# Kernel tuning notes

Hardware: AMD Instinct MI355X
Metric: run time of the kernel (lower is better)

## Reference

```python
import jax, jax.numpy as jnp
import numpy as np

L, H, C = 2, 8, 128          # layers, heads, hidden_channels
D = C // H                   # head dim
NPAT, NICD, NNDC = 50000, 591, 2042
OUT = 90
E = 250000                   # edges per relation
# edge relations as (src_type, dst_type); node types: 0=patient, 1=icd, 2=ndc
ETYPES = [(0, 1), (1, 0), (0, 2), (2, 0)]


def _seg_softmax(logits, seg, n):
    # softmax over edges grouped by destination node (PyG `softmax`)
    m = jax.ops.segment_max(logits, seg, num_segments=n)
    e = jnp.exp(logits - m[seg])
    s = jax.ops.segment_sum(e, seg, num_segments=n)
    return e / s[seg]


def setup_inputs() -> dict:
    key = jax.random.key(0)
    ks = jax.random.split(key, 24)
    s = 1.0 / np.sqrt(C)
    n = lambda k, shape, sc: jax.random.normal(k, shape, dtype=jnp.float32) * sc
    return {
        "x_patient": n(ks[0], (NPAT, C), 1.0),
        "w_in_patient": n(ks[1], (C, C), s),
        "b_in_patient": jnp.zeros((C,), jnp.float32),
        "emb_icd": n(ks[2], (NICD, C), 0.1),
        "emb_ndc": n(ks[3], (NNDC, C), 0.1),
        "kw": n(ks[4], (L, 3, C, C), s), "kb": jnp.zeros((L, 3, C), jnp.float32),
        "qw": n(ks[5], (L, 3, C, C), s), "qb": jnp.zeros((L, 3, C), jnp.float32),
        "vw": n(ks[6], (L, 3, C, C), s), "vb": jnp.zeros((L, 3, C), jnp.float32),
        "aw": n(ks[7], (L, 3, C, C), s), "ab": jnp.zeros((L, 3, C), jnp.float32),
        "skip": jnp.ones((L, 3), jnp.float32),
        "a_rel": n(ks[8], (L, 4, H, D, D), 1.0 / np.sqrt(D)),
        "m_rel": n(ks[9], (L, 4, H, D, D), 1.0 / np.sqrt(D)),
        "p_rel": jnp.ones((L, 4, H), jnp.float32),
        "w_out": n(ks[10], (C, OUT), s),
        "b_out": jnp.zeros((OUT,), jnp.float32),
        "x_icd": jnp.arange(NICD, dtype=jnp.int32),
        "x_ndc": jnp.arange(NNDC, dtype=jnp.int32),
        "src_pi": jax.random.randint(ks[11], (E,), 0, NPAT, dtype=jnp.int32),
        "dst_pi": jax.random.randint(ks[12], (E,), 0, NICD, dtype=jnp.int32),
        "src_ip": jax.random.randint(ks[13], (E,), 0, NICD, dtype=jnp.int32),
        "dst_ip": jax.random.randint(ks[14], (E,), 0, NPAT, dtype=jnp.int32),
        "src_pn": jax.random.randint(ks[15], (E,), 0, NPAT, dtype=jnp.int32),
        "dst_pn": jax.random.randint(ks[16], (E,), 0, NNDC, dtype=jnp.int32),
        "src_np": jax.random.randint(ks[17], (E,), 0, NNDC, dtype=jnp.int32),
        "dst_np": jax.random.randint(ks[18], (E,), 0, NPAT, dtype=jnp.int32),
    }


def reference(x_patient, w_in_patient, b_in_patient, emb_icd, emb_ndc,
              kw, kb, qw, qb, vw, vb, aw, ab, skip,
              a_rel, m_rel, p_rel, w_out, b_out,
              x_icd, x_ndc,
              src_pi, dst_pi, src_ip, dst_ip, src_pn, dst_pn, src_np, dst_np):
    edges = [(src_pi, dst_pi), (src_ip, dst_ip), (src_pn, dst_pn), (src_np, dst_np)]
    sizes = [NPAT, NICD, NNDC]
    # per-type input projection / embedding + relu
    x = [jax.nn.relu(x_patient @ w_in_patient + b_in_patient),
         jax.nn.relu(emb_icd[x_icd]),
         jax.nn.relu(emb_ndc[x_ndc])]
    scale = 1.0 / np.sqrt(D)
    for l in range(L):
        k = [(x[t] @ kw[l, t] + kb[l, t]).reshape(-1, H, D) for t in range(3)]
        q = [(x[t] @ qw[l, t] + qb[l, t]).reshape(-1, H, D) for t in range(3)]
        v = [(x[t] @ vw[l, t] + vb[l, t]).reshape(-1, H, D) for t in range(3)]
        agg = [jnp.zeros((sizes[t], H, D), x[0].dtype) for t in range(3)]
        for r, (st, dt) in enumerate(ETYPES):
            src, dst = edges[r]
            kr = jnp.einsum('nhd,hde->nhe', k[st], a_rel[l, r])  # relation key transform
            vr = jnp.einsum('nhd,hde->nhe', v[st], m_rel[l, r])  # relation msg transform
            alpha = jnp.sum(q[dt][dst] * kr[src], axis=-1) * p_rel[l, r] * scale  # [E,H]
            alpha = _seg_softmax(alpha, dst, sizes[dt])
            agg[dt] = agg[dt] + jax.ops.segment_sum(vr[src] * alpha[:, :, None], dst, num_segments=sizes[dt])
        new_x = []
        for t in range(3):
            o = jax.nn.gelu(agg[t].reshape(-1, C)) @ aw[l, t] + ab[l, t]
            a = jax.nn.sigmoid(skip[l, t])
            new_x.append(a * o + (1.0 - a) * x[t])  # learned skip (dims match)
        x = new_x
    return jax.nn.sigmoid(x[0] @ w_out + b_out)
```

## Files before the change

### kernel.cpp

```cpp
#include <hip/hip_runtime.h>
#include <math.h>

#define CDIM  128
#define NHEAD 8
#define DHEAD 16
#define NPAT  50000
#define NICD  591
#define NNDC  2042
#define OUTN  90
#define NEDGE 250000
#define NLAYER 2
#define ALC   640

#define OFF0  0
#define OFF1  (NICD)
#define OFF2  (NICD + NPAT)
#define OFF3  (NICD + NPAT + NNDC)
#define NTOT  (NICD + NPAT + NNDC + NPAT)

#define LDP 40
#define CTILE 72
#define LOG2E 1.4426950408889634f

typedef __attribute__((ext_vector_type(8))) short bf16x8;
typedef __attribute__((ext_vector_type(4))) float f32x4;

__device__ __forceinline__ float gelu_tanh(float x) {
    float x3 = x * x * x;
    return 0.5f * x * (1.0f + tanhf(0.7978845608028654f * (x + 0.044715f * x3)));
}
__device__ __forceinline__ float b2f(unsigned short u) {
    union { unsigned int i; float f; } v; v.i = ((unsigned int)u) << 16; return v.f;
}
__device__ __forceinline__ unsigned short f2b(float f) {
    union { float ff; unsigned int i; } v; v.ff = f;
    unsigned int i = v.i;
    return (unsigned short)((i + 0x7FFFu + ((i >> 16) & 1u)) >> 16);
}
__device__ __forceinline__ float2 b2x2(unsigned int u) {
    union { unsigned int i; float f; } lo, hi;
    lo.i = u << 16; hi.i = u & 0xFFFF0000u;
    return make_float2(lo.f, hi.f);
}

__global__ __launch_bounds__(256) void gemm_xs(
    const void* __restrict__ Ap, int a_mode, int lda,
    const unsigned short* __restrict__ Wt, const float* __restrict__ bias,
    void* __restrict__ Cp, int c_mode, int ldc,
    int M, int N, int act, int ntile,
    const unsigned short* __restrict__ xold, int ldx,
    const float* __restrict__ skipv, int skipidx)
{
    __shared__ unsigned short Al[64 * LDP];
    __shared__ unsigned short Bl[64 * LDP];
    __shared__ unsigned short Cst[64 * CTILE];
    int nwg = gridDim.x;
    int orig = blockIdx.x;
    int qq = nwg >> 3, rr = nwg & 7;
    int xcd = orig & 7, idx = orig >> 3;
    int wgid = (xcd < rr ? xcd * (qq + 1) : rr * (qq + 1) + (xcd - rr) * qq) + idx;
    int bm = (wgid / ntile) * 64, bn = (wgid % ntile) * 64;

    int t = threadIdx.x;
    int lane = t & 63, w = t >> 6;
    int wr = w >> 1, wc = w & 1;
    int quad = lane >> 4, lm = lane & 15;
    f32x4 acc[2][2] = {};
    const int srow = t >> 2;
    const int skq  = (t & 3) * 8;

    for (int k0 = 0; k0 < 128; k0 += 32) {
        {
            int row = bm + srow;
            uint4 u = make_uint4(0, 0, 0, 0);
            if (a_mode == 0) {
                if (row < M)
                    u = *(const uint4*)((const unsigned short*)Ap + (size_t)row * lda + k0 + skq);
            } else {
                float f[8] = {0.f,0.f,0.f,0.f,0.f,0.f,0.f,0.f};
                if (row < M) {
                    const float4* ap = (const float4*)((const float*)Ap + (size_t)row * lda + k0 + skq);
                    float4 u0 = ap[0], u1 = ap[1];
                    f[0]=u0.x; f[1]=u0.y; f[2]=u0.z; f[3]=u0.w;
                    f[4]=u1.x; f[5]=u1.y; f[6]=u1.z; f[7]=u1.w;
                }
                unsigned short v[8];
                for (int i = 0; i < 8; i++) v[i] = f2b(f[i]);
                u = *(uint4*)v;
            }
            *(uint4*)&Al[srow * LDP + skq] = u;
        }
        {
            int n = bn + srow;
            uint4 u = make_uint4(0, 0, 0, 0);
            if (n < N) u = *(const uint4*)(Wt + (size_t)n * 128 + k0 + skq);
            *(uint4*)&Bl[srow * LDP + skq] = u;
        }
        __syncthreads();
        bf16x8 af[2], bfr[2];
        #pragma unroll
        for (int i = 0; i < 2; i++) {
            af[i]  = *(const bf16x8*)&Al[(wr * 32 + i * 16 + lm) * LDP + quad * 8];
            bfr[i] = *(const bf16x8*)&Bl[(wc * 32 + i * 16 + lm) * LDP + quad * 8];
        }
        acc[0][0] = __builtin_amdgcn_mfma_f32_16x16x32_bf16(af[0], bfr[0], acc[0][0], 0, 0, 0);
        acc[0][1] = __builtin_amdgcn_mfma_f32_16x16x32_bf16(af[0], bfr[1], acc[0][1], 0, 0, 0);
        acc[1][0] = __builtin_amdgcn_mfma_f32_16x16x32_bf16(af[1], bfr[0], acc[1][0], 0, 0, 0);
        acc[1][1] = __builtin_amdgcn_mfma_f32_16x16x32_bf16(af[1], bfr[1], acc[1][1], 0, 0, 0);
        __syncthreads();
    }

    float aSk = 0.f, oneM = 0.f;
    if (skipv) {
        float sv = skipv[skipidx];
        aSk = 1.0f / (1.0f + expf(-sv));
        oneM = 1.0f - aSk;
    }
    if (c_mode == 0) {
        #pragma unroll
        for (int tm = 0; tm < 2; tm++)
        #pragma unroll
        for (int tn = 0; tn < 2; tn++)
        #pragma unroll
        for (int r = 0; r < 4; r++) {
            int lrow = wr * 32 + tm * 16 + quad * 4 + r;
            int lcol = wc * 32 + tn * 16 + lm;
            int row = bm + lrow, col = bn + lcol;
            float v = acc[tm][tn][r] + (bias ? bias[col] : 0.f);
            if (act == 1) v = fmaxf(v, 0.f);
            if (skipv && row < M) v = aSk * v + oneM * b2f(xold[(size_t)row * ldx + col]);
            Cst[lrow * CTILE + lcol] = f2b(v);
        }
        __syncthreads();
        int row = t >> 2, seg = (t & 3) * 16;
        if (bm + row < M) {
            unsigned short* dst = (unsigned short*)Cp + (size_t)(bm + row) * ldc + bn + seg;
            *(uint4*)dst       = *(const uint4*)&Cst[row * CTILE + seg];
            *(uint4*)(dst + 8) = *(const uint4*)&Cst[row * CTILE + seg + 8];
        }
    } else {
        #pragma unroll
        for (int tm = 0; tm < 2; tm++)
        #pragma unroll
        for (int tn = 0; tn < 2; tn++)
        #pragma unroll
        for (int r = 0; r < 4; r++) {
            int row = bm + wr * 32 + tm * 16 + quad * 4 + r;
            int col = bn + wc * 32 + tn * 16 + lm;
            if (row >= M || col >= N) continue;
            float v = acc[tm][tn][r] + (bias ? bias[col] : 0.f);
            if (act == 1) v = fmaxf(v, 0.f);
            else if (act == 2) v = 1.0f / (1.0f + expf(-v));
            ((float*)Cp)[(size_t)row * ldc + col] = v;
        }
    }
}

__global__ __launch_bounds__(256) void wprep_all(
    const float* __restrict__ qw, const float* __restrict__ aw,
    const float* __restrict__ w_in, const float* __restrict__ w_out,
    unsigned short* __restrict__ Wb0, unsigned short* __restrict__ Wb1,
    unsigned short* __restrict__ Wb2, unsigned short* __restrict__ Wtaw,
    unsigned short* __restrict__ Wtin, unsigned short* __restrict__ Wtout)
{
    __shared__ float tile[32][33];
    int z = blockIdx.z;
    const float* s; unsigned short* d; int N = 128;
    if (z < 2)       { s = qw + (size_t)z * 3 * 16384;              d = Wb0 + (size_t)z * 640 * 128; }
    else if (z < 4)  { s = qw + 16384 + (size_t)(z - 2) * 3 * 16384; d = Wb1 + (size_t)(z - 2) * 384 * 128; }
    else if (z < 6)  { s = qw + 2 * 16384 + (size_t)(z - 4) * 3 * 16384; d = Wb2 + (size_t)(z - 4) * 384 * 128; }
    else if (z < 12) { s = aw + (size_t)(z - 6) * 16384;            d = Wtaw + (size_t)(z - 6) * 16384; }
    else if (z == 12){ s = w_in;  d = Wtin; }
    else             { s = w_out; d = Wtout; N = OUTN; }
    int k0 = blockIdx.x * 32, n0 = blockIdx.y * 32;
    int tx = threadIdx.x & 31, ty = threadIdx.x >> 5;
    for (int i = 0; i < 32; i += 8) {
        int k = k0 + ty + i, n = n0 + tx;
        tile[ty + i][tx] = (k < 128 && n < N) ? s[(size_t)k * N + n] : 0.f;
    }
    __syncthreads();
    for (int i = 0; i < 32; i += 8) {
        int n = n0 + ty + i, k = k0 + tx;
        if (n < N && k < 128) d[(size_t)n * 128 + k] = f2b(tile[tx][ty + i]);
    }
}

__global__ __launch_bounds__(256) void wcomp_kernel(
    const float* __restrict__ kw, const float* __restrict__ vw,
    const float* __restrict__ a_rel, const float* __restrict__ m_rel,
    const float* __restrict__ kb, const float* __restrict__ vb,
    unsigned short* __restrict__ Wb0, unsigned short* __restrict__ Wb1,
    unsigned short* __restrict__ Wb2,
    float* __restrict__ bb0, float* __restrict__ bb1, float* __restrict__ bb2)
{
    int s = blockIdx.x;
    int l = s >> 3, j = s & 7;
    int t, isV, r, rowoff, nw;
    unsigned short* Wb; float* bb;
    switch (j) {
      case 0: t=0; isV=0; r=0; Wb=Wb0; bb=bb0; rowoff=128; nw=640; break;
      case 1: t=0; isV=1; r=0; Wb=Wb0; bb=bb0; rowoff=256; nw=640; break;
      case 2: t=0; isV=0; r=2; Wb=Wb0; bb=bb0; rowoff=384; nw=640; break;
      case 3: t=0; isV=1; r=2; Wb=Wb0; bb=bb0; rowoff=512; nw=640; break;
      case 4: t=1; isV=0; r=1; Wb=Wb1; bb=bb1; rowoff=128; nw=384; break;
      case 5: t=1; isV=1; r=1; Wb=Wb1; bb=bb1; rowoff=256; nw=384; break;
      case 6: t=2; isV=0; r=3; Wb=Wb2; bb=bb2; rowoff=128; nw=384; break;
      default:t=2; isV=1; r=3; Wb=Wb2; bb=bb2; rowoff=256; nw=384; break;
    }
    const float* W = (isV ? vw : kw) + (size_t)(l * 3 + t) * 16384;
    const float* A = (isV ? m_rel : a_rel) + (size_t)(l * 4 + r) * 2048;
    const float* B = (isV ? vb : kb) + (size_t)(l * 3 + t) * 128;
    unsigned short* dst = Wb + (size_t)l * nw * 128 + (size_t)rowoff * 128;
    float* bdst = bb + (size_t)l * nw + rowoff;
    int n = threadIdx.x & 127;
    int kh = threadIdx.x >> 7;
    int h = n >> 4, e = n & 15;
    float Ar[16];
    #pragma unroll
    for (int d = 0; d < 16; d++) Ar[d] = A[h * 256 + d * 16 + e];
    for (int k = kh * 64; k < kh * 64 + 64; k++) {
        float acc = 0.f;
        const float* wr = W + (size_t)k * 128 + h * 16;
        #pragma unroll
        for (int d = 0; d < 16; d++) acc += wr[d] * Ar[d];
        dst[(size_t)n * 128 + k] = f2b(acc);
    }
    if (kh == 0) {
        float acc = 0.f;
        const float* br = B + h * 16;
        #pragma unroll
        for (int d = 0; d < 16; d++) acc += br[d] * Ar[d];
        bdst[n] = acc;
    }
}

__global__ void biasq_kernel(const float* __restrict__ qb,
                             float* __restrict__ bb0, float* __restrict__ bb1,
                             float* __restrict__ bb2) {
    int t = blockIdx.x * blockDim.x + threadIdx.x;
    if (t >= 6 * 128) return;
    int g = t >> 7, c = t & 127;
    int l = g / 3, ty = g % 3;
    float v = qb[g * 128 + c];
    if (ty == 0) bb0[l * 640 + c] = v;
    else if (ty == 1) bb1[l * 384 + c] = v;
    else bb2[l * 384 + c] = v;
}

__global__ __launch_bounds__(256) void hist4_kernel(
    const int* __restrict__ d0, const int* __restrict__ d1,
    const int* __restrict__ d2, const int* __restrict__ d3,
    int* __restrict__ deg)
{
    __shared__ int lh[2048];
    int rel = blockIdx.y;
    int t = threadIdx.x;
    const int* dp = (rel == 0) ? d0 : (rel == 1) ? d1 : (rel == 2) ? d2 : d3;
    int off = (rel == 0) ? OFF0 : (rel == 1) ? OFF1 : (rel == 2) ? OFF2 : OFF3;
    if (rel == 1 || rel == 3) {
        for (int e = blockIdx.x * 256 + t; e < NEDGE; e += gridDim.x * 256)
            atomicAdd(&deg[off + dp[e]], 1);
    } else {
        int nb = (rel == 0) ? NICD : NNDC;
        for (int i = t; i < nb; i += 256) lh[i] = 0;
        __syncthreads();
        for (int e = blockIdx.x * 256 + t; e < NEDGE; e += gridDim.x * 256)
            atomicAdd(&lh[dp[e]], 1);
        __syncthreads();
        for (int i = t; i < nb; i += 256) {
            int v = lh[i];
            if (v) atomicAdd(&deg[off + i], v);
        }
    }
}

__global__ __launch_bounds__(256) void scanA_kernel(
    const int* __restrict__ deg, int* __restrict__ part, int n)
{
    __shared__ int red[256];
    int b = blockIdx.x, t = threadIdx.x;
    int base = b * 1024 + t * 4;
    int s = 0;
    if (base + 3 < n) {
        int4 v = *(const int4*)(deg + base);
        s = v.x + v.y + v.z + v.w;
    } else {
        for (int i = 0; i < 4; i++) if (base + i < n) s += deg[base + i];
    }
    red[t] = s;
    __syncthreads();
    for (int o = 128; o; o >>= 1) { if (t < o) red[t] += red[t + o]; __syncthreads(); }
    if (t == 0) part[b] = red[0];
}

__global__ __launch_bounds__(128) void scanB_kernel(int* __restrict__ part, int nb)
{
    __shared__ int s[256];
    int t = threadIdx.x;
    for (int i = t; i < nb; i += 128) s[i] = part[i];
    __syncthreads();
    if (t == 0) { int run = 0; for (int i = 0; i < nb; i++) { int v = s[i]; s[i] = run; run += v; } }
    __syncthreads();
    for (int i = t; i < nb; i += 128) part[i] = s[i];
}

__global__ __launch_bounds__(256) void scanC_kernel(
    const int* __restrict__ deg, const int* __restrict__ part,
    int* __restrict__ rp0, int* __restrict__ rp1,
    int* __restrict__ rp2, int* __restrict__ rp3,
    int* __restrict__ cursor, int n)
{
    __shared__ int red[256];
    int b = blockIdx.x, t = threadIdx.x;
    int base = b * 1024 + t * 4;
    int v[4] = {0, 0, 0, 0};
    if (base + 3 < n) {
        int4 q = *(const int4*)(deg + base);
        v[0] = q.x; v[1] = q.y; v[2] = q.z; v[3] = q.w;
    } else {
        for (int i = 0; i < 4; i++) if (base + i < n) v[i] = deg[base + i];
    }
    red[t] = v[0] + v[1] + v[2] + v[3];
    __syncthreads();
    for (int off = 1; off < 256; off <<= 1) {
        int y = (t >= off) ? red[t - off] : 0;
        __syncthreads();
        red[t] += y;
        __syncthreads();
    }
    int run = part[b] + ((t == 0) ? 0 : red[t - 1]);
    for (int i = 0; i < 4; i++) {
        int g = base + i;
        if (g < n) {
            cursor[g] = run;
            int r, loc;
            if      (g < OFF1) { r = 0; loc = g; }
            else if (g < OFF2) { r = 1; loc = g - OFF1; }
            else if (g < OFF3) { r = 2; loc = g - OFF2; }
            else               { r = 3; loc = g - OFF3; }
            int Sl = run - r * NEDGE;
            ((r == 0) ? rp0 : (r == 1) ? rp1 : (r == 2) ? rp2 : rp3)[loc] = Sl;
            run += v[i];
        }
    }
    if (b == 0 && t == 0) {
        rp0[NICD] = NEDGE; rp1[NPAT] = NEDGE; rp2[NNDC] = NEDGE; rp3[NPAT] = NEDGE;
    }
}

__global__ __launch_bounds__(256) void scatter_pack_kernel(
    const int* __restrict__ s0, const int* __restrict__ d0,
    const int* __restrict__ s1, const int* __restrict__ d1,
    const int* __restrict__ s2, const int* __restrict__ d2,
    const int* __restrict__ s3, const int* __restrict__ d3,
    int* __restrict__ cursor, unsigned int* __restrict__ es)
{
    __shared__ int lcnt[2048];
    __shared__ int lbase[2048];
    int rel = blockIdx.y;
    int t = threadIdx.x;
    const int* sp = (rel == 0) ? s0 : (rel == 1) ? s1 : (rel == 2) ? s2 : s3;
    const int* dp = (rel == 0) ? d0 : (rel == 1) ? d1 : (rel == 2) ? d2 : d3;
    int off = (rel == 0) ? OFF0 : (rel == 1) ? OFF1 : (rel == 2) ? OFF2 : OFF3;
    if (rel == 1 || rel == 3) {
        for (int e = blockIdx.x * 256 + t; e < NEDGE; e += gridDim.x * 256) {
            int d = dp[e];
            int p = atomicAdd(&cursor[off + d], 1);
            es[p] = ((unsigned int)sp[e] << 16) | (unsigned int)d;
        }
    } else {
        int nb = (rel == 0) ? NICD : NNDC;
        int per = (NEDGE + gridDim.x - 1) / gridDim.x;
        int e0 = blockIdx.x * per, e1 = min(e0 + per, NEDGE);
        for (int i = t; i < nb; i += 256) lcnt[i] = 0;
        __syncthreads();
        for (int e = e0 + t; e < e1; e += 256) atomicAdd(&lcnt[dp[e]], 1);
        __syncthreads();
        for (int i = t; i < nb; i += 256) {
            int c = lcnt[i];
            lbase[i] = c ? atomicAdd(&cursor[off + i], c) : 0;
            lcnt[i] = 0;
        }
        __syncthreads();
        for (int e = e0 + t; e < e1; e += 256) {
            int d = dp[e];
            int p = lbase[d] + atomicAdd(&lcnt[d], 1);
            es[p] = ((unsigned int)sp[e] << 16) | (unsigned int)d;
        }
    }
}

__global__ void gather_relu2_kernel(
    const float* __restrict__ embA, const int* __restrict__ idxA,
    unsigned short* __restrict__ outA, int nA,
    const float* __restrict__ embB, const int* __restrict__ idxB,
    unsigned short* __restrict__ outB, int nB)
{
    int t = blockIdx.x * blockDim.x + threadIdx.x;
    int totA = nA * CDIM;
    if (t < totA) {
        int r = t >> 7, c = t & 127;
        outA[t] = f2b(fmaxf(embA[(size_t)idxA[r] * CDIM + c], 0.f));
    } else if (t < totA + nB * CDIM) {
        int u = t - totA;
        int r = u >> 7, c = u & 127;
        outB[u] = f2b(fmaxf(embB[(size_t)idxB[r] * CDIM + c], 0.f));
    }
}

__device__ __forceinline__ float dot16_bf(const unsigned short* a,
                                          const unsigned short* b) {
    const uint4* ap = (const uint4*)a;
    const uint4* bp = (const uint4*)b;
    uint4 a0 = ap[0], a1 = ap[1], b0 = bp[0], b1 = bp[1];
    unsigned int au[8] = {a0.x, a0.y, a0.z, a0.w, a1.x, a1.y, a1.z, a1.w};
    unsigned int bu[8] = {b0.x, b0.y, b0.z, b0.w, b1.x, b1.y, b1.z, b1.w};
    float acc = 0.f;
    #pragma unroll
    for (int j = 0; j < 8; j++) {
        float2 x = b2x2(au[j]), y = b2x2(bu[j]);
        acc += x.x * y.x + x.y * y.y;
    }
    return acc;
}

__device__ __forceinline__ float dot16_q(uint4 a0, uint4 a1,
                                         const unsigned short* b) {
    const uint4* bp = (const uint4*)b;
    uint4 b0 = bp[0], b1 = bp[1];
    unsigned int au[8] = {a0.x, a0.y, a0.z, a0.w, a1.x, a1.y, a1.z, a1.w};
    unsigned int bu[8] = {b0.x, b0.y, b0.z, b0.w, b1.x, b1.y, b1.z, b1.w};
    float acc = 0.f;
    #pragma unroll
    for (int j = 0; j < 8; j++) {
        float2 x = b2x2(au[j]), y = b2x2(bu[j]);
        acc += x.x * y.x + x.y * y.y;
    }
    return acc;
}

__global__ __launch_bounds__(256) void seg_fused_kernel(
    const int* __restrict__ rpA, const unsigned int* __restrict__ esA,
    const unsigned short* __restrict__ qA, int ldqA,
    const unsigned short* __restrict__ krA, const unsigned short* __restrict__ vrA, int ldsA,
    const float* __restrict__ prelA, float* __restrict__ alphaA,
    unsigned short* __restrict__ aggA, int ndA,
    const int* __restrict__ rpB, const unsigned int* __restrict__ esB,
    const unsigned short* __restrict__ qB, int ldqB,
    const unsigned short* __restrict__ krB, const unsigned short* __restrict__ vrB, int ldsB,
    const float* __restrict__ prelB, float* __restrict__ alphaB,
    unsigned short* __restrict__ aggB, int ndB)
{
    __shared__ float wred[4][8];
    __shared__ float sinv[8];
    __shared__ float p3f[4][64][2];
    __shared__ float wl[ALC * NHEAD];
    __shared__ unsigned short sl[ALC];
    int rel = blockIdx.y;
    int n = blockIdx.x;
    const int* rp            = rel ? rpB : rpA;
    const unsigned int* es   = rel ? esB : esA;
    const unsigned short* q  = rel ? qB : qA;
    int ldq                  = rel ? ldqB : ldqA;
    const unsigned short* kr = rel ? krB : krA;
    const unsigned short* vr = rel ? vrB : vrA;
    int ldsrc                = rel ? ldsB : ldsA;
    const float* prel        = rel ? prelB : prelA;
    float* alpha             = rel ? alphaB : alphaA;
    unsigned short* agg      = rel ? aggB : aggA;
    int nd                   = rel ? ndB : ndA;
    if (n >= nd) return;

    int r0 = rp[n], deg = rp[n + 1] - r0;
    int t = threadIdx.x;
    int h = t & 7, j = t >> 3;
    int lane = t & 63, wv = t >> 6;
    const unsigned short* qrow = q + (size_t)n * ldq + h * DHEAD;
    uint4 qa = ((const uint4*)qrow)[0], qb = ((const uint4*)qrow)[1];
    float ph = prel[h] * 0.25f * LOG2E;

    if (deg <= ALC) {
        for (int i = t; i < deg; i += 256) sl[i] = (unsigned short)(es[r0 + i] >> 16);
        __syncthreads();

        float mx = -1e30f;
        int i = j;
        for (; i + 96 < deg; i += 128) {
            int s0 = sl[i], s1 = sl[i + 32], s2 = sl[i + 64], s3 = sl[i + 96];
            float a0 = dot16_q(qa, qb, kr + (size_t)s0 * ldsrc + h * DHEAD) * ph;
            float a1 = dot16_q(qa, qb, kr + (size_t)s1 * ldsrc + h * DHEAD) * ph;
            float a2 = dot16_q(qa, qb, kr + (size_t)s2 * ldsrc + h * DHEAD) * ph;
            float a3 = dot16_q(qa, qb, kr + (size_t)s3 * ldsrc + h * DHEAD) * ph;
            wl[(i)      * NHEAD + h] = a0;
            wl[(i + 32) * NHEAD + h] = a1;
            wl[(i + 64) * NHEAD + h] = a2;
            wl[(i + 96) * NHEAD + h] = a3;
            mx = fmaxf(mx, fmaxf(fmaxf(a0, a1), fmaxf(a2, a3)));
        }
        for (; i < deg; i += 32) {
            int s0 = sl[i];
            float a = dot16_q(qa, qb, kr + (size_t)s0 * ldsrc + h * DHEAD) * ph;
            wl[i * NHEAD + h] = a;
            mx = fmaxf(mx, a);
        }
        mx = fmaxf(mx, __shfl_xor(mx, 8));
        mx = fmaxf(mx, __shfl_xor(mx, 16));
        mx = fmaxf(mx, __shfl_xor(mx, 32));
        if (lane < 8) wred[wv][h] = mx;
        __syncthreads();
        float m = fmaxf(fmaxf(wred[0][h], wred[1][h]), fmaxf(wred[2][h], wred[3][h]));
        __syncthreads();

        float sm = 0.f;
        for (i = j; i < deg; i += 32) {
            float e = exp2f(wl[i * NHEAD + h] - m);
            wl[i * NHEAD + h] = e;
            sm += e;
        }
        sm += __shfl_xor(sm, 8);
        sm += __shfl_xor(sm, 16);
        sm += __shfl_xor(sm, 32);
        if (lane < 8) wred[wv][h] = sm;
        __syncthreads();
        if (t < 8) {
            float s = wred[0][t] + wred[1][t] + wred[2][t] + wred[3][t];
            sinv[t] = (s > 0.f) ? 1.0f / s : 0.f;
        }
        __syncthreads();

        int g = t >> 6, l = t & 63;
        int hh = l >> 3;
        float acc0 = 0.f, acc1 = 0.f;
        i = g;
        for (; i + 28 < deg; i += 32) {
            int e0 = sl[i],      e1 = sl[i + 4],  e2 = sl[i + 8],  e3 = sl[i + 12];
            int e4 = sl[i + 16], e5 = sl[i + 20], e6 = sl[i + 24], e7 = sl[i + 28];
            unsigned int u0 = *(const unsigned int*)(vr + (size_t)e0 * ldsrc + 2 * l);
            unsigned int u1 = *(const unsigned int*)(vr + (size_t)e1 * ldsrc + 2 * l);
            unsigned int u2 = *(const unsigned int*)(vr + (size_t)e2 * ldsrc + 2 * l);
            unsigned int u3 = *(const unsigned int*)(vr + (size_t)e3 * ldsrc + 2 * l);
            unsigned int u4 = *(const unsigned int*)(vr + (size_t)e4 * ldsrc + 2 * l);
            unsigned int u5 = *(const unsigned int*)(vr + (size_t)e5 * ldsrc + 2 * l);
            unsigned int u6 = *(const unsigned int*)(vr + (size_t)e6 * ldsrc + 2 * l);
            unsigned int u7 = *(const unsigned int*)(vr + (size_t)e7 * ldsrc + 2 * l);
            float w0 = wl[(i)      * NHEAD + hh], w1 = wl[(i + 4)  * NHEAD + hh];
            float w2 = wl[(i + 8)  * NHEAD + hh], w3 = wl[(i + 12) * NHEAD + hh];
            float w4 = wl[(i + 16) * NHEAD + hh], w5 = wl[(i + 20) * NHEAD + hh];
            float w6 = wl[(i + 24) * NHEAD + hh], w7 = wl[(i + 28) * NHEAD + hh];
            float2 v0 = b2x2(u0), v1 = b2x2(u1), v2 = b2x2(u2), v3 = b2x2(u3);
            float2 v4 = b2x2(u4), v5 = b2x2(u5), v6 = b2x2(u6), v7 = b2x2(u7);
            acc0 += w0 * v0.x + w1 * v1.x + w2 * v2.x + w3 * v3.x
                  + w4 * v4.x + w5 * v5.x + w6 * v6.x + w7 * v7.x;
            acc1 += w0 * v0.y + w1 * v1.y + w2 * v2.y + w3 * v3.y
                  + w4 * v4.y + w5 * v5.y + w6 * v6.y + w7 * v7.y;
        }
        for (; i < deg; i += 4) {
            int e0 = sl[i];
            unsigned int u0 = *(const unsigned int*)(vr + (size_t)e0 * ldsrc + 2 * l);
            float w0 = wl[i * NHEAD + hh];
            float2 v0 = b2x2(u0);
            acc0 += w0 * v0.x;
            acc1 += w0 * v0.y;
        }
        p3f[g][l][0] = acc0;
        p3f[g][l][1] = acc1;
        __syncthreads();
        if (t < 128) {
            int c = t;
            float v = p3f[0][c >> 1][c & 1] + p3f[1][c >> 1][c & 1]
                    + p3f[2][c >> 1][c & 1] + p3f[3][c >> 1][c & 1];
            agg[(size_t)n * CDIM + c] = f2b(gelu_tanh(v * sinv[c >> 4]));
        }
    } else {
        float* p3 = (float*)p3f;
        float mx = -1e30f;
        for (int i = j; i < deg; i += 32) {
            int sn = es[r0 + i] >> 16;
            float a = dot16_q(qa, qb, kr + (size_t)sn * ldsrc + h * DHEAD) * ph;
            alpha[(size_t)(r0 + i) * NHEAD + h] = a;
            mx = fmaxf(mx, a);
        }
        mx = fmaxf(mx, __shfl_xor(mx, 8));
        mx = fmaxf(mx, __shfl_xor(mx, 16));
        mx = fmaxf(mx, __shfl_xor(mx, 32));
        if (lane < 8) wred[wv][h] = mx;
        __syncthreads();
        float m = fmaxf(fmaxf(wred[0][h], wred[1][h]), fmaxf(wred[2][h], wred[3][h]));
        __syncthreads();

        float sm = 0.f;
        for (int i = j; i < deg; i += 32) {
            size_t ai = (size_t)(r0 + i) * NHEAD + h;
            float e = exp2f(alpha[ai] - m);
            alpha[ai] = e;
            sm += e;
        }
        sm += __shfl_xor(sm, 8);
        sm += __shfl_xor(sm, 16);
        sm += __shfl_xor(sm, 32);
        if (lane < 8) wred[wv][h] = sm;
        __syncthreads();
        if (t < 8) {
            float s = wred[0][t] + wred[1][t] + wred[2][t] + wred[3][t];
            sinv[t] = (s > 0.f) ? 1.0f / s : 0.f;
        }
        __syncthreads();

        int c = t & 127, half = t >> 7;
        float hsi = sinv[c >> 4];
        float acc = 0.f;
        int i = half;
        for (; i + 6 < deg; i += 8) {
            unsigned int e0 = es[r0 + i],     e1 = es[r0 + i + 2];
            unsigned int e2 = es[r0 + i + 4], e3 = es[r0 + i + 6];
            float w0 = alpha[(size_t)(r0 + i)     * NHEAD + (c >> 4)];
            float w1 = alpha[(size_t)(r0 + i + 2) * NHEAD + (c >> 4)];
            float w2 = alpha[(size_t)(r0 + i + 4) * NHEAD + (c >> 4)];
            float w3 = alpha[(size_t)(r0 + i + 6) * NHEAD + (c >> 4)];
            float v0 = b2f(vr[(size_t)(e0 >> 16) * ldsrc + c]);
            float v1 = b2f(vr[(size_t)(e1 >> 16) * ldsrc + c]);
            float v2 = b2f(vr[(size_t)(e2 >> 16) * ldsrc + c]);
            float v3 = b2f(vr[(size_t)(e3 >> 16) * ldsrc + c]);
            acc += w0 * v0 + w1 * v1 + w2 * v2 + w3 * v3;
        }
        for (; i < deg; i += 2) {
            unsigned int e0 = es[r0 + i];
            float w0 = alpha[(size_t)(r0 + i) * NHEAD + (c >> 4)];
            acc += w0 * b2f(vr[(size_t)(e0 >> 16) * ldsrc + c]);
        }
        p3[t] = acc * hsi;
        __syncthreads();
        if (half == 0) agg[(size_t)n * CDIM + c] = f2b(gelu_tanh(p3[c] + p3[128 + c]));
    }
}

__global__ __launch_bounds__(256) void edge_softmax_agg2_kernel(
    const int* __restrict__ rp1, const unsigned int* __restrict__ es1,
    const int* __restrict__ rp3, const unsigned int* __restrict__ es3,
    const unsigned short* __restrict__ q, int ldq,
    const unsigned short* __restrict__ kr1, const unsigned short* __restrict__ vr1, int ld1,
    const unsigned short* __restrict__ kr3, const unsigned short* __restrict__ vr3, int ld3,
    const float* __restrict__ prel1, const float* __restrict__ prel3,
    unsigned short* __restrict__ agg, int nd)
{
    __shared__ float wls[4][128 * NHEAD];
    __shared__ int slo[4][128];
    int wv  = threadIdx.x >> 6;
    int wid = (blockIdx.x * 256 + threadIdx.x) >> 6;
    int lane = threadIdx.x & 63;
    if (wid >= nd) return;
    float* wl = wls[wv];
    int* sl = slo[wv];
    int h = lane & 7, j = lane >> 3;
    int hc = lane >> 3;
    const unsigned short* qbase = q + (size_t)wid * ldq;
    float acc0 = 0.f, acc1 = 0.f;

    int r0a = rp1[wid], degA = rp1[wid + 1] - r0a;
    int r0b = rp3[wid], degB = rp3[wid + 1] - r0b;

    if (degA <= 64 && degB <= 64) {
        const unsigned short* qrow = qbase + h * DHEAD;
        float phA = prel1[h] * 0.25f * LOG2E;
        float phB = prel3[h] * 0.25f * LOG2E;
        int dOfs = (int)(kr3 - kr1);
        float mA = -1e30f, mB = -1e30f;
        for (int i = j; i < degA; i += 8) {
            int sn = es1[r0a + i] >> 16;
            int off = sn * ld1;
            float a = dot16_bf(qrow, kr1 + off + h * DHEAD) * phA;
            wl[i * NHEAD + h] = a;
            if (h == 0) sl[i] = off;
            mA = fmaxf(mA, a);
        }
        for (int i = j; i < degB; i += 8) {
            int sn = es3[r0b + i] >> 16;
            int off = sn * ld3;
            float a = dot16_bf(qrow, kr3 + off + h * DHEAD) * phB;
            wl[(degA + i) * NHEAD + h] = a;
            if (h == 0) sl[degA + i] = dOfs + off;
            mB = fmaxf(mB, a);
        }
        mA = fmaxf(mA, __shfl_xor(mA, 8));   mB = fmaxf(mB, __shfl_xor(mB, 8));
        mA = fmaxf(mA, __shfl_xor(mA, 16));  mB = fmaxf(mB, __shfl_xor(mB, 16));
        mA = fmaxf(mA, __shfl_xor(mA, 32));  mB = fmaxf(mB, __shfl_xor(mB, 32));

        int dtot = degA + degB;
        float sA = 0.f, sB = 0.f;
        for (int i = j; i < dtot; i += 8) {
            bool isA = i < degA;
            float e = exp2f(wl[i * NHEAD + h] - (isA ? mA : mB));
            wl[i * NHEAD + h] = e;
            sA += isA ? e : 0.f;
            sB += isA ? 0.f : e;
        }
        sA += __shfl_xor(sA, 8);   sB += __shfl_xor(sB, 8);
        sA += __shfl_xor(sA, 16);  sB += __shfl_xor(sB, 16);
        sA += __shfl_xor(sA, 32);  sB += __shfl_xor(sB, 32);
        float siA = (sA > 0.f) ? 1.0f / sA : 0.f;
        float siB = (sB > 0.f) ? 1.0f / sB : 0.f;
        for (int i = j; i < dtot; i += 8)
            wl[i * NHEAD + h] *= (i < degA) ? siA : siB;

        int i = 0;
        for (; i + 4 <= dtot; i += 4) {
            int o0 = sl[i + 0], o1 = sl[i + 1], o2 = sl[i + 2], o3 = sl[i + 3];
            unsigned int u0 = *(const unsigned int*)(vr1 + o0 + 2 * lane);
            unsigned int u1 = *(const unsigned int*)(vr1 + o1 + 2 * lane);
            unsigned int u2 = *(const unsigned int*)(vr1 + o2 + 2 * lane);
            unsigned int u3 = *(const unsigned int*)(vr1 + o3 + 2 * lane);
            float w0 = wl[(i + 0) * NHEAD + hc];
            float w1 = wl[(i + 1) * NHEAD + hc];
            float w2 = wl[(i + 2) * NHEAD + hc];
            float w3 = wl[(i + 3) * NHEAD + hc];
            float2 v0 = b2x2(u0), v1 = b2x2(u1), v2 = b2x2(u2), v3 = b2x2(u3);
            acc0 += w0 * v0.x + w1 * v1.x + w2 * v2.x + w3 * v3.x;
            acc1 += w0 * v0.y + w1 * v1.y + w2 * v2.y + w3 * v3.y;
        }
        for (; i < dtot; i++) {
            int o0 = sl[i];
            unsigned int u0 = *(const unsigned int*)(vr1 + o0 + 2 * lane);
            float w0 = wl[i * NHEAD + hc];
            float2 v0 = b2x2(u0);
            acc0 += w0 * v0.x; acc1 += w0 * v0.y;
        }
    } else {
        #pragma unroll
        for (int rr = 0; rr < 2; rr++) {
            const unsigned int* es = rr ? es3 : es1;
            const unsigned short* kr = rr ? kr3 : kr1;
            const unsigned short* vr = rr ? vr3 : vr1;
            int ld = rr ? ld3 : ld1;
            const float* prel = rr ? prel3 : prel1;
            int r0 = rr ? r0b : r0a;
            int deg = rr ? degB : degA;
            if (deg <= 0) continue;
            const unsigned short* qrow = qbase + h * DHEAD;
            float ph = prel[h] * 0.25f * LOG2E;
            bool small = (deg <= 64);

            float m = -1e30f;
            for (int i = j; i < deg; i += 8) {
                int sn = es[r0 + i] >> 16;
                float a = dot16_bf(qrow, kr + (size_t)sn * ld + h * DHEAD) * ph;
                if (small) wl[i * NHEAD + h] = a;
                m = fmaxf(m, a);
            }
            m = fmaxf(m, __shfl_xor(m, 8));
            m = fmaxf(m, __shfl_xor(m, 16));
            m = fmaxf(m, __shfl_xor(m, 32));
            float s = 0.f;
            for (int i = j; i < deg; i += 8) {
                float a;
                if (small) a = wl[i * NHEAD + h];
                else {
                    int sn = es[r0 + i] >> 16;
                    a = dot16_bf(qrow, kr + (size_t)sn * ld + h * DHEAD) * ph;
                }
                float e = exp2f(a - m);
                if (small) wl[i * NHEAD + h] = e;
                s += e;
            }
            s += __shfl_xor(s, 8);
            s += __shfl_xor(s, 16);
            s += __shfl_xor(s, 32);
            float si = (s > 0.f) ? 1.0f / s : 0.f;
            if (small)
                for (int i = j; i < deg; i += 8)
                    wl[i * NHEAD + h] *= si;

            float m_hc  = __shfl(m, hc);
            float si_hc = __shfl(si, hc);
            float ph_hc = __shfl(ph, hc);
            const unsigned short* qrow_hc = qbase + hc * DHEAD;
            for (int i = 0; i < deg; i++) {
                unsigned int sv = es[r0 + i] >> 16;
                unsigned int pv = *(const unsigned int*)(vr + (size_t)sv * ld + 2 * lane);
                float2 v = b2x2(pv);
                float wgt;
                if (small) wgt = wl[i * NHEAD + hc];
                else {
                    float a = dot16_bf(qrow_hc, kr + (size_t)sv * ld + hc * DHEAD) * ph_hc;
                    wgt = exp2f(a - m_hc) * si_hc;
                }
                acc0 += wgt * v.x;
                acc1 += wgt * v.y;
            }
        }
    }
    unsigned int packed = (unsigned int)f2b(gelu_tanh(acc0))
                        | ((unsigned int)f2b(gelu_tanh(acc1)) << 16);
    *(unsigned int*)(agg + (size_t)wid * CDIM + 2 * lane) = packed;
}

extern "C" void kernel_launch(void* const* d_in, const int* in_sizes, int n_in,
                              void* d_out, int out_size, void* d_ws, size_t ws_size,
                              hipStream_t stream)
{
    const float* x_patient = (const float*)d_in[0];
    const float* w_in      = (const float*)d_in[1];
    const float* b_in      = (const float*)d_in[2];
    const float* emb_icd   = (const float*)d_in[3];
    const float* emb_ndc   = (const float*)d_in[4];
    const float* kw        = (const float*)d_in[5];
    const float* kbias     = (const float*)d_in[6];
    const float* qw        = (const float*)d_in[7];
    const float* qbias     = (const float*)d_in[8];
    const float* vw        = (const float*)d_in[9];
    const float* vbias     = (const float*)d_in[10];
    const float* aw        = (const float*)d_in[11];
    const float* abias     = (const float*)d_in[12];
    const float* skip      = (const float*)d_in[13];
    const float* a_rel     = (const float*)d_in[14];
    const float* m_rel     = (const float*)d_in[15];
    const float* p_rel     = (const float*)d_in[16];
    const float* w_out     = (const float*)d_in[17];
    const float* b_out     = (const float*)d_in[18];
    const int*   x_icd     = (const int*)d_in[19];
    const int*   x_ndc     = (const int*)d_in[20];
    const int* esrc[4] = {(const int*)d_in[21], (const int*)d_in[23],
                          (const int*)d_in[25], (const int*)d_in[27]};
    const int* edst[4] = {(const int*)d_in[22], (const int*)d_in[24],
                          (const int*)d_in[26], (const int*)d_in[28]};

    const int sizes[3] = {NPAT, NICD, NNDC};

    char* p = (char*)d_ws;
    auto alloc = [&](size_t bytes) -> void* {
        void* r = (void*)p;
        p += (bytes + 255) & ~(size_t)255;
        return r;
    };

    unsigned short *xb[3];
    for (int t = 0; t < 3; t++) xb[t] = (unsigned short*)alloc((size_t)sizes[t] * CDIM * 2);
    unsigned short* P0 = (unsigned short*)alloc((size_t)NPAT * 640 * 2);
    unsigned short* P1 = (unsigned short*)alloc((size_t)NICD * 384 * 2);
    unsigned short* P2 = (unsigned short*)alloc((size_t)NNDC * 384 * 2);
    unsigned short* aggbase = (unsigned short*)alloc((size_t)(NPAT + NICD + NNDC) * CDIM * 2);
    unsigned short* agg[3];
    agg[0] = aggbase;
    agg[1] = aggbase + (size_t)NPAT * CDIM;
    agg[2] = agg[1] + (size_t)NICD * CDIM;
    float*  alphabuf  = (float*)alloc((size_t)NEDGE * NHEAD * 4);
    float*  alphabuf2 = (float*)alloc((size_t)NEDGE * NHEAD * 4);
    unsigned int* esbig = (unsigned int*)alloc((size_t)4 * NEDGE * 4);
    int* rowptr[4];
    rowptr[0] = (int*)alloc((size_t)(NICD + 1) * 4);
    rowptr[1] = (int*)alloc((size_t)(NPAT + 1) * 4);
    rowptr[2] = (int*)alloc((size_t)(NNDC + 1) * 4);
    rowptr[3] = (int*)alloc((size_t)(NPAT + 1) * 4);
    int* deg    = (int*)alloc((size_t)NTOT * 4);
    int* cursor = (int*)alloc((size_t)NTOT * 4);
    int* part   = (int*)alloc((size_t)256 * 4);
    unsigned short* Wb0   = (unsigned short*)alloc((size_t)2 * 640 * 128 * 2);
    unsigned short* Wb1   = (unsigned short*)alloc((size_t)2 * 384 * 128 * 2);
    unsigned short* Wb2   = (unsigned short*)alloc((size_t)2 * 384 * 128 * 2);
    unsigned short* Wtaw  = (unsigned short*)alloc((size_t)6 * 128 * 128 * 2);
    unsigned short* Wtin  = (unsigned short*)alloc((size_t)128 * 128 * 2);
    unsigned short* Wtout = (unsigned short*)alloc((size_t)OUTN * 128 * 2);
    float* bb0 = (float*)alloc((size_t)2 * 640 * 4);
    float* bb1 = (float*)alloc((size_t)2 * 384 * 4);
    float* bb2 = (float*)alloc((size_t)2 * 384 * 4);
    unsigned int* esRel[4];
    for (int r = 0; r < 4; r++) esRel[r] = esbig + (size_t)r * NEDGE;

    auto gemm = [&](const void* A, int a_mode, int lda,
                    const unsigned short* Wt, const float* bias,
                    void* C, int c_mode, int ldc, int M, int N, int act,
                    const unsigned short* xold, int ldx,
                    const float* skipv, int skipidx) {
        int ntile = (N + 63) / 64;
        int nwg = ((M + 63) / 64) * ntile;
        gemm_xs<<<dim3(nwg), dim3(256), 0, stream>>>(A, a_mode, lda, Wt, bias,
            C, c_mode, ldc, M, N, act, ntile, xold, ldx, skipv, skipidx);
    };

    wprep_all<<<dim3(4, 4, 14), 256, 0, stream>>>(qw, aw, w_in, w_out,
        Wb0, Wb1, Wb2, Wtaw, Wtin, Wtout);
    wcomp_kernel<<<16, 256, 0, stream>>>(kw, vw, a_rel, m_rel, kbias, vbias,
        Wb0, Wb1, Wb2, bb0, bb1, bb2);
    biasq_kernel<<<3, 256, 0, stream>>>(qbias, bb0, bb1, bb2);

    {
        const int NB = (NTOT + 1023) / 1024;
        hipMemsetAsync(deg, 0, (size_t)NTOT * 4, stream);
        hist4_kernel<<<dim3(64, 4), 256, 0, stream>>>(
            edst[0], edst[1], edst[2], edst[3], deg);
        scanA_kernel<<<NB, 256, 0, stream>>>(deg, part, NTOT);
        scanB_kernel<<<1, 128, 0, stream>>>(part, NB);
        scanC_kernel<<<NB, 256, 0, stream>>>(deg, part,
            rowptr[0], rowptr[1], rowptr[2], rowptr[3], cursor, NTOT);
        scatter_pack_kernel<<<dim3(64, 4), 256, 0, stream>>>(
            esrc[0], edst[0], esrc[1], edst[1], esrc[2], edst[2], esrc[3], edst[3],
            cursor, esbig);
    }

    gemm(x_patient, 1, 128, Wtin, b_in, xb[0], 0, 128, NPAT, 128, 1, nullptr, 0, nullptr, 0);
    gather_relu2_kernel<<<((NICD + NNDC) * CDIM + 255) / 256, 256, 0, stream>>>(
        emb_icd, x_icd, xb[1], NICD, emb_ndc, x_ndc, xb[2], NNDC);

    for (int l = 0; l < NLAYER; l++) {
        gemm(xb[0], 0, 128, Wb0 + (size_t)l * 640 * 128, bb0 + (size_t)l * 640,
             P0, 0, 640, NPAT, 640, 0, nullptr, 0, nullptr, 0);
        gemm(xb[1], 0, 128, Wb1 + (size_t)l * 384 * 128, bb1 + (size_t)l * 384,
             P1, 0, 384, NICD, 384, 0, nullptr, 0, nullptr, 0);
        gemm(xb[2], 0, 128, Wb2 + (size_t)l * 384 * 128, bb2 + (size_t)l * 384,
             P2, 0, 384, NNDC, 384, 0, nullptr, 0, nullptr, 0);

        seg_fused_kernel<<<dim3(NNDC, 2), 256, 0, stream>>>(
            rowptr[0], esRel[0], P1, 384, P0 + 128, P0 + 256, 640,
            p_rel + (size_t)(l * 4 + 0) * NHEAD, alphabuf, agg[1], NICD,
            rowptr[2], esRel[2], P2, 384, P0 + 384, P0 + 512, 640,
            p_rel + (size_t)(l * 4 + 2) * NHEAD, alphabuf2, agg[2], NNDC);

        edge_softmax_agg2_kernel<<<(NPAT + 3) / 4, 256, 0, stream>>>(
            rowptr[1], esRel[1], rowptr[3], esRel[3],
            P0, 640, P1 + 128, P1 + 256, 384, P2 + 128, P2 + 256, 384,
            p_rel + (size_t)(l * 4 + 1) * NHEAD, p_rel + (size_t)(l * 4 + 3) * NHEAD,
            agg[0], NPAT);

        for (int t = 0; t < 3; t++) {
            int wi = l * 3 + t;
            gemm(agg[t], 0, 128, Wtaw + (size_t)wi * 128 * 128, abias + (size_t)wi * 128,
                 xb[t], 0, 128, sizes[t], 128, 0, xb[t], 128, skip, wi);
        }
    }

    gemm(xb[0], 0, 128, Wtout, b_out, d_out, 1, OUTN, NPAT, OUTN, 2, nullptr, 0, nullptr, 0);
}
```

Baseline: 559.9 us.

## Merge per-type GEMMs and edge kernels into combined multi-task launches

Groups the three per-node-type projection GEMMs into one launch, and likewise the three post-aggregation skip GEMMs, using block-index ranges to pick the problem. The two edge-attention kernels are merged into one launch that shares a single static shared-memory buffer. This cuts launch count and lets small-node-type work overlap with the large patient work instead of leaving the GPU idle at kernel tails. The cost is a union shared-memory footprint per block, which can lower occupancy for the lighter branch, and the XCD remap now applies only to the first sub-problem.

```diff
diff --git a/kernel.cpp b/kernel.cpp
--- a/kernel.cpp
+++ b/kernel.cpp
@@ -22,6 +22,9 @@
 #define CTILE 72
 #define LOG2E 1.4426950408889634f
 
+#define NSEG  (2 * NNDC)
+#define NAGG  ((NPAT + 3) / 4)
+
 typedef __attribute__((ext_vector_type(8))) short bf16x8;
 typedef __attribute__((ext_vector_type(4))) float f32x4;
 
@@ -41,6 +44,111 @@
     union { unsigned int i; float f; } lo, hi;
     lo.i = u << 16; hi.i = u & 0xFFFF0000u;
     return make_float2(lo.f, hi.f);
+}
+
+__device__ __forceinline__ void gemm_core(
+    const unsigned short* __restrict__ Ap,
+    const unsigned short* __restrict__ Wt, const float* __restrict__ bias,
+    unsigned short* __restrict__ Cp, int ldc,
+    int M, int N, int ntile, int wgid,
+    const unsigned short* __restrict__ xold,
+    const float* __restrict__ skipv, int skipidx,
+    unsigned short* Al, unsigned short* Bl, unsigned short* Cst)
+{
+    int bm = (wgid / ntile) * 64, bn = (wgid % ntile) * 64;
+    int t = threadIdx.x;
+    int lane = t & 63, w = t >> 6;
+    int wr = w >> 1, wc = w & 1;
+    int quad = lane >> 4, lm = lane & 15;
+    f32x4 acc[2][2] = {};
+    const int srow = t >> 2;
+    const int skq  = (t & 3) * 8;
+
+    for (int k0 = 0; k0 < 128; k0 += 32) {
+        {
+            int row = bm + srow;
+            uint4 u = make_uint4(0, 0, 0, 0);
+            if (row < M)
+                u = *(const uint4*)(Ap + (size_t)row * 128 + k0 + skq);
+            *(uint4*)&Al[srow * LDP + skq] = u;
+        }
+        {
+            int n = bn + srow;
+            uint4 u = make_uint4(0, 0, 0, 0);
+            if (n < N) u = *(const uint4*)(Wt + (size_t)n * 128 + k0 + skq);
+            *(uint4*)&Bl[srow * LDP + skq] = u;
+        }
+        __syncthreads();
+        bf16x8 af[2], bfr[2];
+        #pragma unroll
+        for (int i = 0; i < 2; i++) {
+            af[i]  = *(const bf16x8*)&Al[(wr * 32 + i * 16 + lm) * LDP + quad * 8];
+            bfr[i] = *(const bf16x8*)&Bl[(wc * 32 + i * 16 + lm) * LDP + quad * 8];
+        }
+        acc[0][0] = __builtin_amdgcn_mfma_f32_16x16x32_bf16(af[0], bfr[0], acc[0][0], 0, 0, 0);
+        acc[0][1] = __builtin_amdgcn_mfma_f32_16x16x32_bf16(af[0], bfr[1], acc[0][1], 0, 0, 0);
+        acc[1][0] = __builtin_amdgcn_mfma_f32_16x16x32_bf16(af[1], bfr[0], acc[1][0], 0, 0, 0);
+        acc[1][1] = __builtin_amdgcn_mfma_f32_16x16x32_bf16(af[1], bfr[1], acc[1][1], 0, 0, 0);
+        __syncthreads();
+    }
+
+    float aSk = 0.f, oneM = 0.f;
+    if (skipv) {
+        float sv = skipv[skipidx];
+        aSk = 1.0f / (1.0f + expf(-sv));
+        oneM = 1.0f - aSk;
+    }
+    #pragma unroll
+    for (int tm = 0; tm < 2; tm++)
+    #pragma unroll
+    for (int tn = 0; tn < 2; tn++)
+    #pragma unroll
+    for (int r = 0; r < 4; r++) {
+        int lrow = wr * 32 + tm * 16 + quad * 4 + r;
+        int lcol = wc * 32 + tn * 16 + lm;
+        int row = bm + lrow, col = bn + lcol;
+        float v = acc[tm][tn][r] + (bias ? bias[col] : 0.f);
+        if (skipv && row < M) v = aSk * v + oneM * b2f(xold[(size_t)row * ldc + col]);
+        Cst[lrow * CTILE + lcol] = f2b(v);
+    }
+    __syncthreads();
+    int row = t >> 2, seg = (t & 3) * 16;
+    if (bm + row < M) {
+        unsigned short* dst = Cp + (size_t)(bm + row) * ldc + bn + seg;
+        *(uint4*)dst       = *(const uint4*)&Cst[row * CTILE + seg];
+        *(uint4*)(dst + 8) = *(const uint4*)&Cst[row * CTILE + seg + 8];
+    }
+}
+
+__global__ __launch_bounds__(256) void gemm3_kernel(
+    const unsigned short* __restrict__ A0, const unsigned short* __restrict__ W0,
+    const float* __restrict__ b0, unsigned short* __restrict__ C0,
+    int M0, int N0, int ntile0, int nwg0,
+    const unsigned short* __restrict__ A1, const unsigned short* __restrict__ W1,
+    const float* __restrict__ b1, unsigned short* __restrict__ C1,
+    int M1, int N1, int ntile1, int nwg01,
+    const unsigned short* __restrict__ A2, const unsigned short* __restrict__ W2,
+    const float* __restrict__ b2, unsigned short* __restrict__ C2,
+    int M2, int N2, int ntile2,
+    const float* __restrict__ skipv, int si0, int si1, int si2)
+{
+    __shared__ unsigned short Al[64 * LDP];
+    __shared__ unsigned short Bl[64 * LDP];
+    __shared__ unsigned short Cst[64 * CTILE];
+    int b = blockIdx.x;
+    if (b < nwg0) {
+        int qq = nwg0 >> 3, rr = nwg0 & 7;
+        int xcd = b & 7, idx = b >> 3;
+        int wgid = (xcd < rr ? xcd * (qq + 1) : rr * (qq + 1) + (xcd - rr) * qq) + idx;
+        gemm_core(A0, W0, b0, C0, N0, M0, N0, ntile0, wgid,
+                  C0, skipv, si0, Al, Bl, Cst);
+    } else if (b < nwg01) {
+        gemm_core(A1, W1, b1, C1, N1, M1, N1, ntile1, b - nwg0,
+                  C1, skipv, si1, Al, Bl, Cst);
+    } else {
+        gemm_core(A2, W2, b2, C2, N2, M2, N2, ntile2, b - nwg01,
+                  C2, skipv, si2, Al, Bl, Cst);
+    }
 }
 
 __global__ __launch_bounds__(256) void gemm_xs(
@@ -110,12 +218,6 @@
         __syncthreads();
     }
 
-    float aSk = 0.f, oneM = 0.f;
-    if (skipv) {
-        float sv = skipv[skipidx];
-        aSk = 1.0f / (1.0f + expf(-sv));
-        oneM = 1.0f - aSk;
-    }
     if (c_mode == 0) {
         #pragma unroll
         for (int tm = 0; tm < 2; tm++)
@@ -125,10 +227,9 @@
         for (int r = 0; r < 4; r++) {
             int lrow = wr * 32 + tm * 16 + quad * 4 + r;
             int lcol = wc * 32 + tn * 16 + lm;
-            int row = bm + lrow, col = bn + lcol;
+            int col = bn + lcol;
             float v = acc[tm][tn][r] + (bias ? bias[col] : 0.f);
             if (act == 1) v = fmaxf(v, 0.f);
-            if (skipv && row < M) v = aSk * v + oneM * b2f(xold[(size_t)row * ldx + col]);
             Cst[lrow * CTILE + lcol] = f2b(v);
         }
         __syncthreads();
@@ -439,7 +540,8 @@
     return acc;
 }
 
-__global__ __launch_bounds__(256) void seg_fused_kernel(
+__device__ void seg_body(
+    int rel, int n, char* smem,
     const int* __restrict__ rpA, const unsigned int* __restrict__ esA,
     const unsigned short* __restrict__ qA, int ldqA,
     const unsigned short* __restrict__ krA, const unsigned short* __restrict__ vrA, int ldsA,
@@ -451,13 +553,12 @@
     const float* __restrict__ prelB, float* __restrict__ alphaB,
     unsigned short* __restrict__ aggB, int ndB)
 {
-    __shared__ float wred[4][8];
-    __shared__ float sinv[8];
-    __shared__ float p3f[4][64][2];
-    __shared__ float wl[ALC * NHEAD];
-    __shared__ unsigned short sl[ALC];
-    int rel = blockIdx.y;
-    int n = blockIdx.x;
+    float (*wred)[8] = (float(*)[8])smem;
+    float* sinv = (float*)(smem + 128);
+    float (*p3f)[64][2] = (float(*)[64][2])(smem + 160);
+    float* wl = (float*)(smem + 2208);
+    unsigned short* sl = (unsigned short*)(smem + 22688);
+
     const int* rp            = rel ? rpB : rpA;
     const unsigned int* es   = rel ? esB : esA;
     const unsigned short* q  = rel ? qB : qA;
@@ -634,7 +735,8 @@
     }
 }
 
-__global__ __launch_bounds__(256) void edge_softmax_agg2_kernel(
+__device__ void agg2_body(
+    int lb, char* smem,
     const int* __restrict__ rp1, const unsigned int* __restrict__ es1,
     const int* __restrict__ rp3, const unsigned int* __restrict__ es3,
     const unsigned short* __restrict__ q, int ldq,
@@ -643,14 +745,14 @@
     const float* __restrict__ prel1, const float* __restrict__ prel3,
     unsigned short* __restrict__ agg, int nd)
 {
-    __shared__ float wls[4][128 * NHEAD];
-    __shared__ int slo[4][128];
+    float* wls = (float*)smem;
+    int* slo = (int*)(smem + 16384);
     int wv  = threadIdx.x >> 6;
-    int wid = (blockIdx.x * 256 + threadIdx.x) >> 6;
+    int wid = lb * 4 + wv;
     int lane = threadIdx.x & 63;
     if (wid >= nd) return;
-    float* wl = wls[wv];
-    int* sl = slo[wv];
+    float* wl = wls + wv * 128 * NHEAD;
+    int* sl = slo + wv * 128;
     int h = lane & 7, j = lane >> 3;
     int hc = lane >> 3;
     const unsigned short* qbase = q + (size_t)wid * ldq;
@@ -791,6 +893,38 @@
     unsigned int packed = (unsigned int)f2b(gelu_tanh(acc0))
                         | ((unsigned int)f2b(gelu_tanh(acc1)) << 16);
     *(unsigned int*)(agg + (size_t)wid * CDIM + 2 * lane) = packed;
+}
+
+__global__ __launch_bounds__(256) void edge_all_kernel(
+    const int* __restrict__ rpA, const unsigned int* __restrict__ esA,
+    const unsigned short* __restrict__ qA, int ldqA,
+    const unsigned short* __restrict__ krA, const unsigned short* __restrict__ vrA, int ldsA,
+    const float* __restrict__ prelA, float* __restrict__ alphaA,
+    unsigned short* __restrict__ aggA, int ndA,
+    const int* __restrict__ rpB, const unsigned int* __restrict__ esB,
+    const unsigned short* __restrict__ qB, int ldqB,
+    const unsigned short* __restrict__ krB, const unsigned short* __restrict__ vrB, int ldsB,
+    const float* __restrict__ prelB, float* __restrict__ alphaB,
+    unsigned short* __restrict__ aggB, int ndB,
+    const int* __restrict__ rp1, const unsigned int* __restrict__ es1,
+    const int* __restrict__ rp3, const unsigned int* __restrict__ es3,
+    const unsigned short* __restrict__ qP, int ldqP,
+    const unsigned short* __restrict__ kr1, const unsigned short* __restrict__ vr1, int ld1,
+    const unsigned short* __restrict__ kr3, const unsigned short* __restrict__ vr3, int ld3,
+    const float* __restrict__ prel1, const float* __restrict__ prel3,
+    unsigned short* __restrict__ aggP, int ndP)
+{
+    __shared__ __align__(16) char smem[23968];
+    int b = blockIdx.x;
+    if (b < NSEG) {
+        seg_body(b & 1, b >> 1, smem,
+                 rpA, esA, qA, ldqA, krA, vrA, ldsA, prelA, alphaA, aggA, ndA,
+                 rpB, esB, qB, ldqB, krB, vrB, ldsB, prelB, alphaB, aggB, ndB);
+    } else {
+        agg2_body(b - NSEG, smem,
+                  rp1, es1, rp3, es3, qP, ldqP, kr1, vr1, ld1, kr3, vr3, ld3,
+                  prel1, prel3, aggP, ndP);
+    }
 }
 
 extern "C" void kernel_launch(void* const* d_in, const int* in_sizes, int n_in,
@@ -865,17 +999,6 @@
     unsigned int* esRel[4];
     for (int r = 0; r < 4; r++) esRel[r] = esbig + (size_t)r * NEDGE;
 
-    auto gemm = [&](const void* A, int a_mode, int lda,
-                    const unsigned short* Wt, const float* bias,
-                    void* C, int c_mode, int ldc, int M, int N, int act,
-                    const unsigned short* xold, int ldx,
-                    const float* skipv, int skipidx) {
-        int ntile = (N + 63) / 64;
-        int nwg = ((M + 63) / 64) * ntile;
-        gemm_xs<<<dim3(nwg), dim3(256), 0, stream>>>(A, a_mode, lda, Wt, bias,
-            C, c_mode, ldc, M, N, act, ntile, xold, ldx, skipv, skipidx);
-    };
-
     wprep_all<<<dim3(4, 4, 14), 256, 0, stream>>>(qw, aw, w_in, w_out,
         Wb0, Wb1, Wb2, Wtaw, Wtin, Wtout);
     wcomp_kernel<<<16, 256, 0, stream>>>(kw, vw, a_rel, m_rel, kbias, vbias,
@@ -896,36 +1019,57 @@
             cursor, esbig);
     }
 
-    gemm(x_patient, 1, 128, Wtin, b_in, xb[0], 0, 128, NPAT, 128, 1, nullptr, 0, nullptr, 0);
+    {
+        int ntile = 2;
+        int nwg = ((NPAT + 63) / 64) * ntile;
+        gemm_xs<<<dim3(nwg), dim3(256), 0, stream>>>(x_patient, 1, 128, Wtin, b_in,
+            xb[0], 0, 128, NPAT, 128, 1, ntile, nullptr, 0, nullptr, 0);
+    }
     gather_relu2_kernel<<<((NICD + NNDC) * CDIM + 255) / 256, 256, 0, stream>>>(
         emb_icd, x_icd, xb[1], NICD, emb_ndc, x_ndc, xb[2], NNDC);
 
+    const int ntP0 = 640 / 64, nwgP0 = ((NPAT + 63) / 64) * ntP0;
+    const int ntP1 = 384 / 64, nwgP1 = ((NICD + 63) / 64) * ntP1;
+    const int ntP2 = 384 / 64, nwgP2 = ((NNDC + 63) / 64) * ntP2;
+    const int ntS  = 128 / 64;
+    const int nwgS0 = ((NPAT + 63) / 64) * ntS;
+    const int nwgS1 = ((NICD + 63) / 64) * ntS;
+    const int nwgS2 = ((NNDC + 63) / 64) * ntS;
+
     for (int l = 0; l < NLAYER; l++) {
-        gemm(xb[0], 0, 128, Wb0 + (size_t)l * 640 * 128, bb0 + (size_t)l * 640,
-             P0, 0, 640, NPAT, 640, 0, nullptr, 0, nullptr, 0);
-        gemm(xb[1], 0, 128, Wb1 + (size_t)l * 384 * 128, bb1 + (size_t)l * 384,
-             P1, 0, 384, NICD, 384, 0, nullptr, 0, nullptr, 0);
-        gemm(xb[2], 0, 128, Wb2 + (size_t)l * 384 * 128, bb2 + (size_t)l * 384,
-             P2, 0, 384, NNDC, 384, 0, nullptr, 0, nullptr, 0);
-
-        seg_fused_kernel<<<dim3(NNDC, 2), 256, 0, stream>>>(
+        gemm3_kernel<<<dim3(nwgP0 + nwgP1 + nwgP2), dim3(256), 0, stream>>>(
+            xb[0], Wb0 + (size_t)l * 640 * 128, bb0 + (size_t)l * 640, P0,
+            NPAT, 640, ntP0, nwgP0,
+            xb[1], Wb1 + (size_t)l * 384 * 128, bb1 + (size_t)l * 384, P1,
+            NICD, 384, ntP1, nwgP0 + nwgP1,
+            xb[2], Wb2 + (size_t)l * 384 * 128, bb2 + (size_t)l * 384, P2,
+            NNDC, 384, ntP2,
+            nullptr, 0, 0, 0);
+
+        edge_all_kernel<<<dim3(NSEG + NAGG), dim3(256), 0, stream>>>(
             rowptr[0], esRel[0], P1, 384, P0 + 128, P0 + 256, 640,
             p_rel + (size_t)(l * 4 + 0) * NHEAD, alphabuf, agg[1], NICD,
             rowptr[2], esRel[2], P2, 384, P0 + 384, P0 + 512, 640,
-            p_rel + (size_t)(l * 4 + 2) * NHEAD, alphabuf2, agg[2], NNDC);
-
-        edge_softmax_agg2_kernel<<<(NPAT + 3) / 4, 256, 0, stream>>>(
+            p_rel + (size_t)(l * 4 + 2) * NHEAD, alphabuf2, agg[2], NNDC,
             rowptr[1], esRel[1], rowptr[3], esRel[3],
             P0, 640, P1 + 128, P1 + 256, 384, P2 + 128, P2 + 256, 384,
             p_rel + (size_t)(l * 4 + 1) * NHEAD, p_rel + (size_t)(l * 4 + 3) * NHEAD,
             agg[0], NPAT);
 
-        for (int t = 0; t < 3; t++) {
-            int wi = l * 3 + t;
-            gemm(agg[t], 0, 128, Wtaw + (size_t)wi * 128 * 128, abias + (size_t)wi * 128,
-                 xb[t], 0, 128, sizes[t], 128, 0, xb[t], 128, skip, wi);
-        }
-    }
-
-    gemm(xb[0], 0, 128, Wtout, b_out, d_out, 1, OUTN, NPAT, OUTN, 2, nullptr, 0, nullptr, 0);
-}
+        gemm3_kernel<<<dim3(nwgS0 + nwgS1 + nwgS2), dim3(256), 0, stream>>>(
+            agg[0], Wtaw + (size_t)(l * 3 + 0) * 16384, abias + (size_t)(l * 3 + 0) * 128, xb[0],
+            NPAT, 128, ntS, nwgS0,
+            agg[1], Wtaw + (size_t)(l * 3 + 1) * 16384, abias + (size_t)(l * 3 + 1) * 128, xb[1],
+            NICD, 128, ntS, nwgS0 + nwgS1,
+            agg[2], Wtaw + (size_t)(l * 3 + 2) * 16384, abias + (size_t)(l * 3 + 2) * 128, xb[2],
+            NNDC, 128, ntS,
+            skip, l * 3 + 0, l * 3 + 1, l * 3 + 2);
+    }
+
+    {
+        int ntile = (OUTN + 63) / 64;
+        int nwg = ((NPAT + 63) / 64) * ntile;
+        gemm_xs<<<dim3(nwg), dim3(256), 0, stream>>>(xb[0], 0, 128, Wtout, b_out,
+            d_out, 1, OUTN, NPAT, OUTN, 2, ntile, nullptr, 0, nullptr, 0);
+    }
+}
```

Measured after the change: 526.7 us. 5.9% less time.
